# Optimization experiments

Measured on AMD Instinct MI355X. Metric: run time of the kernel, lower is better.

Reference implementation:

```python
import jax, jax.numpy as jnp
import numpy as np

DIRECTIONS = [(0, 0), (1, 0), (-1, 0), (0, 1), (0, -1)]  # (dx, dy)
BN_EPS = 1e-5


def shift2d(x, directions=DIRECTIONS):
    # x: (B, C, H, W). Split channels into G groups, roll each spatially,
    # zero out the wrapped-around border (zero_pad mode), then concat.
    C = x.shape[1]
    G = len(directions)
    base = C // G
    sizes = [base] * (G - 1) + [C - base * (G - 1)]
    starts = np.concatenate([[0], np.cumsum(sizes)])
    out = []
    for i, (dx, dy) in enumerate(directions):
        chunk = x[:, starts[i]:starts[i + 1]]
        if dx == 0 and dy == 0:
            out.append(chunk)
            continue
        y = jnp.roll(chunk, shift=(dy, dx), axis=(-2, -1))
        if dy > 0:
            y = y.at[..., :dy, :].set(0.0)
        elif dy < 0:
            y = y.at[..., dy:, :].set(0.0)
        if dx > 0:
            y = y.at[..., :, :dx].set(0.0)
        elif dx < 0:
            y = y.at[..., :, dx:].set(0.0)
        out.append(y)
    return jnp.concatenate(out, axis=1)


def setup_inputs() -> dict:
    key = jax.random.key(0)
    k1, k2, k3, k4 = jax.random.split(key, 4)
    B, Cin, Cout, H, W = 32, 256, 256, 56, 56
    x = jax.random.normal(k1, (B, Cin, H, W), dtype=jnp.float32)
    pw_w = jax.random.normal(k2, (Cout, Cin), dtype=jnp.float32) * (1.0 / np.sqrt(Cin))
    gamma = jnp.ones((Cout,), dtype=jnp.float32)
    beta = jnp.zeros((Cout,), dtype=jnp.float32)
    running_mean = jax.random.normal(k3, (Cout,), dtype=jnp.float32) * 0.1
    running_var = jax.random.uniform(k4, (Cout,), dtype=jnp.float32, minval=0.5, maxval=1.5)
    return {"x": x, "pw_w": pw_w, "gamma": gamma, "beta": beta,
            "running_mean": running_mean, "running_var": running_var}


def reference(x, pw_w, gamma, beta, running_mean, running_var):
    # Shift (parameter-free spatial mixing)
    y = shift2d(x)
    # stride=1 -> down is Identity
    # 1x1 conv (no bias): pointwise channel mixing
    y = jnp.einsum('bchw,oc->bohw', y, pw_w)
    # BatchNorm2d (inference form with running stats) + ReLU
    inv = gamma * jax.lax.rsqrt(running_var + BN_EPS)
    y = y * inv[None, :, None, None] + (beta - running_mean * inv)[None, :, None, None]
    return jax.nn.relu(y)
```

## Files before the change

kernel.cpp:

```cpp
#include <hip/hip_runtime.h>

#define H_ 56
#define W_ 56
#define HW_ 3136
#define CIN_ 256
#define COUT_ 256

typedef __attribute__((ext_vector_type(8))) short short8;
typedef __attribute__((ext_vector_type(4))) float f32x4;

__device__ unsigned short g_wbf[COUT_ * CIN_];

__device__ __forceinline__ unsigned short f2bf(float f) {
  union { float f; unsigned int i; } v; v.f = f;
  unsigned int b = v.i + (0x7fffu + ((v.i >> 16) & 1u));
  return (unsigned short)(b >> 16);
}

__global__ __launch_bounds__(256)
void prep_weights(const float* __restrict__ wgt) {
  int idx  = blockIdx.x * 256 + threadIdx.x;
  int j    = idx & 7;
  int lane = (idx >> 3) & 63;
  int b    = (idx >> 9) & 3;
  int ks   = (idx >> 11) & 7;
  int wo   = (idx >> 14) & 1;
  int bo   = idx >> 15;
  int o = bo * 128 + wo * 64 + b * 16 + (lane & 15);
  int k = ks * 32 + j * 4 + (lane >> 4);
  g_wbf[idx] = f2bf(wgt[o * CIN_ + k]);
}

__global__ __launch_bounds__(256, 4)
void shiftconv_gemm(const float* __restrict__ x,
                    const float* __restrict__ gamma,
                    const float* __restrict__ beta,
                    const float* __restrict__ rmean,
                    const float* __restrict__ rvar,
                    float* __restrict__ out)
{
  __shared__ float bnp[256];
  __shared__ float tbuf[4][32 * 33];

  const int t = threadIdx.x;
  const int orig = blockIdx.x;
  const int wgid = (orig & 7) * 392 + (orig >> 3);
  const int bo   = wgid & 1;
  const int bn   = wgid >> 1;

  const int lane = t & 63;
  const int wv   = t >> 6;
  const int wn   = wv & 1;
  const int wo   = wv >> 1;
  const int quad = lane >> 4;
  const int l15  = lane & 15;

  if (t < 128) {
    int o = bo * 128 + t;
    float inv = gamma[o] * rsqrtf(rvar[o] + 1e-5f);
    bnp[2 * t]     = inv;
    bnp[2 * t + 1] = beta[o] - rmean[o] * inv;
  }
  __syncthreads();

  const int nglob0 = bn * 64;
  const int bidx   = nglob0 / HW_;
  const int rem    = nglob0 - bidx * HW_;
  const int hw0    = rem + wn * 32 + l15;
  const int hh0    = hw0 / W_;
  const int ww0    = hw0 - hh0 * W_;
  const int hw1    = hw0 + 16;
  const int hh1    = hw1 / W_;
  const int ww1    = hw1 - hh1 * W_;

  const int qh = quad * HW_;
  const unsigned int base0 = (unsigned int)((hw0 + qh) * 4);
  const unsigned int base1 = (unsigned int)((hw1 + qh) * 4);
  const bool v0L = (ww0 >= 1),      v1L = (ww1 >= 1);
  const bool v0R = (ww0 <= W_ - 2), v1R = (ww1 <= W_ - 2);
  const bool v0U = (hh0 >= 1),      v1U = (hh1 >= 1);
  const bool v0D = (hh0 <= H_ - 2), v1D = (hh1 <= H_ - 2);
  unsigned int vo0[5], vo1[5];
  vo0[0] = base0;                                               vo1[0] = base1;
  vo0[1] = v0L ? (unsigned int)((hw0 - 1  + qh) * 4) : base0;   vo1[1] = v1L ? (unsigned int)((hw1 - 1  + qh) * 4) : base1;
  vo0[2] = v0R ? (unsigned int)((hw0 + 1  + qh) * 4) : base0;   vo1[2] = v1R ? (unsigned int)((hw1 + 1  + qh) * 4) : base1;
  vo0[3] = v0U ? (unsigned int)((hw0 - W_ + qh) * 4) : base0;   vo1[3] = v1U ? (unsigned int)((hw1 - W_ + qh) * 4) : base1;
  vo0[4] = v0D ? (unsigned int)((hw0 + W_ + qh) * 4) : base0;   vo1[4] = v1D ? (unsigned int)((hw1 + W_ + qh) * 4) : base1;
  float fm0[5], fm1[5];
  fm0[0] = 1.f;               fm1[0] = 1.f;
  fm0[1] = v0L ? 1.f : 0.f;   fm1[1] = v1L ? 1.f : 0.f;
  fm0[2] = v0R ? 1.f : 0.f;   fm1[2] = v1R ? 1.f : 0.f;
  fm0[3] = v0U ? 1.f : 0.f;   fm1[3] = v1U ? 1.f : 0.f;
  fm0[4] = v0D ? 1.f : 0.f;   fm1[4] = v1D ? 1.f : 0.f;

  const char* __restrict__ px = (const char*)(x + (size_t)bidx * CIN_ * HW_);
  const unsigned short* __restrict__ wp =
      g_wbf + (size_t)(bo * 2 + wo) * 16384 + lane * 8;

  f32x4 acc[2][4];
  #pragma unroll
  for (int a = 0; a < 2; ++a)
    #pragma unroll
    for (int b = 0; b < 4; ++b)
      acc[a][b] = (f32x4){0.f, 0.f, 0.f, 0.f};

  #pragma unroll
  for (int ks = 0; ks < 8; ++ks) {
    short8 wf[4];
    #pragma unroll
    for (int b = 0; b < 4; ++b)
      wf[b] = *(const short8*)(wp + ks * 2048 + b * 512);

    float fa0[8], fa1[8];
    #pragma unroll
    for (int j = 0; j < 8; ++j) {
      const int c0 = ks * 32 + 4 * j;
      unsigned int o0, o1; float m0, m1;
      if (c0 == 48)       { bool hi = quad >= 3;
        o0 = hi ? vo0[1] : vo0[0]; o1 = hi ? vo1[1] : vo1[0];
        m0 = hi ? fm0[1] : 1.f;    m1 = hi ? fm1[1] : 1.f; }
      else if (c0 == 100) { bool hi = quad >= 2;
        o0 = hi ? vo0[2] : vo0[1]; o1 = hi ? vo1[2] : vo1[1];
        m0 = hi ? fm0[2] : fm0[1]; m1 = hi ? fm1[2] : fm1[1]; }
      else if (c0 == 152) { bool hi = quad >= 1;
        o0 = hi ? vo0[3] : vo0[2]; o1 = hi ? vo1[3] : vo1[2];
        m0 = hi ? fm0[3] : fm0[2]; m1 = hi ? fm1[3] : fm1[2]; }
      else {
        const int r = (c0 >= 51) + (c0 >= 102) + (c0 >= 153) + (c0 >= 204);
        o0 = vo0[r]; o1 = vo1[r]; m0 = fm0[r]; m1 = fm1[r];
      }
      const unsigned int cb = (unsigned int)(c0 * HW_ * 4);
      float v0 = *(const float*)(px + (o0 + cb));
      float v1 = *(const float*)(px + (o1 + cb));
      fa0[j] = v0 * m0;
      fa1[j] = v1 * m1;
    }

    union { short8 v; unsigned int d[4]; } af0, af1;
    #pragma unroll
    for (int jj = 0; jj < 4; ++jj) {
      asm("v_cvt_pk_bf16_f32 %0, %1, %2" : "=v"(af0.d[jj]) : "v"(fa0[2*jj]), "v"(fa0[2*jj+1]));
      asm("v_cvt_pk_bf16_f32 %0, %1, %2" : "=v"(af1.d[jj]) : "v"(fa1[2*jj]), "v"(fa1[2*jj+1]));
    }

    #pragma unroll
    for (int b = 0; b < 4; ++b) {
      acc[0][b] = __builtin_amdgcn_mfma_f32_16x16x32_bf16(af0.v, wf[b], acc[0][b], 0, 0, 0);
      acc[1][b] = __builtin_amdgcn_mfma_f32_16x16x32_bf16(af1.v, wf[b], acc[1][b], 0, 0, 0);
    }
  }

  float invb[4], addb[4];
  #pragma unroll
  for (int b = 0; b < 4; ++b) {
    int ol = wo * 64 + b * 16 + l15;
    invb[b] = bnp[2 * ol];
    addb[b] = bnp[2 * ol + 1];
  }
  float* tb = &tbuf[wv][0];
  const size_t obase0 = (size_t)bidx * COUT_ * HW_;
  #pragma unroll
  for (int hb = 0; hb < 2; ++hb) {
    #pragma unroll
    for (int bb = 0; bb < 2; ++bb) {
      const int b = hb * 2 + bb;
      #pragma unroll
      for (int a = 0; a < 2; ++a)
        #pragma unroll
        for (int r = 0; r < 4; ++r) {
          float v = fmaxf(fmaf(acc[a][b][r], invb[b], addb[b]), 0.f);
          tb[(bb * 16 + l15) * 33 + (a * 16 + quad * 4 + r)] = v;
        }
    }
    asm volatile("s_waitcnt lgkmcnt(0)" ::: "memory");
    #pragma unroll
    for (int oi = 0; oi < 16; ++oi) {
      int ol  = oi * 2 + (lane >> 5);
      int nl  = lane & 31;
      float v = tb[ol * 33 + nl];
      int og  = bo * 128 + wo * 64 + hb * 32 + ol;
      int hwg = rem + wn * 32 + nl;
      out[obase0 + (size_t)og * HW_ + hwg] = v;
    }
    asm volatile("s_waitcnt lgkmcnt(0)" ::: "memory");
  }
}

extern "C" void kernel_launch(void* const* d_in, const int* in_sizes, int n_in,
                              void* d_out, int out_size, void* d_ws, size_t ws_size,
                              hipStream_t stream) {
  const float* x     = (const float*)d_in[0];
  const float* wgt   = (const float*)d_in[1];
  const float* gamma = (const float*)d_in[2];
  const float* beta  = (const float*)d_in[3];
  const float* rmean = (const float*)d_in[4];
  const float* rvar  = (const float*)d_in[5];
  float* out = (float*)d_out;

  prep_weights<<<dim3(256), dim3(256), 0, stream>>>(wgt);
  shiftconv_gemm<<<dim3(3136), dim3(256), 0, stream>>>(x, gamma, beta, rmean, rvar, out);
}
```

Measured before the change: 231.7 us.

## Stage block weight slice in LDS and double spatial tile per 512-thread block

Each block now covers 128 output channels by 128 spatial positions with 8 waves instead of 64 positions with 4 waves. The 64KB bf16 weight slice is loaded once per block into shared memory using direct global-to-LDS loads, replacing per-wave global weight reads inside the K loop. Tiles may now span batch boundaries, so each lane computes its own batch index. The epilogue transpose buffer reuses the weight LDS region. The cost is 64KB+ of LDS per block, which limits occupancy, plus an extra barrier.

```diff
diff --git a/kernel.cpp b/kernel.cpp
--- a/kernel.cpp
+++ b/kernel.cpp
@@ -17,21 +17,26 @@
   return (unsigned short)(b >> 16);
 }
 
+__device__ __forceinline__ void gload_lds16(const unsigned short* g, unsigned short* l) {
+  __builtin_amdgcn_global_load_lds(
+      (const __attribute__((address_space(1))) unsigned int*)g,
+      (__attribute__((address_space(3))) unsigned int*)l, 16, 0, 0);
+}
+
 __global__ __launch_bounds__(256)
 void prep_weights(const float* __restrict__ wgt) {
   int idx  = blockIdx.x * 256 + threadIdx.x;
   int j    = idx & 7;
   int lane = (idx >> 3) & 63;
-  int b    = (idx >> 9) & 3;
-  int ks   = (idx >> 11) & 7;
-  int wo   = (idx >> 14) & 1;
-  int bo   = idx >> 15;
-  int o = bo * 128 + wo * 64 + b * 16 + (lane & 15);
+  int obg  = (idx >> 9) & 7;
+  int ks   = (idx >> 12) & 7;
+  int bm   = idx >> 15;
+  int o = bm * 128 + obg * 16 + (lane & 15);
   int k = ks * 32 + j * 4 + (lane >> 4);
   g_wbf[idx] = f2bf(wgt[o * CIN_ + k]);
 }
 
-__global__ __launch_bounds__(256, 4)
+__global__ __launch_bounds__(512, 4)
 void shiftconv_gemm(const float* __restrict__ x,
                     const float* __restrict__ gamma,
                     const float* __restrict__ beta,
@@ -39,53 +44,55 @@
                     const float* __restrict__ rvar,
                     float* __restrict__ out)
 {
+  __shared__ unsigned short Wlds[128 * 256];
   __shared__ float bnp[256];
-  __shared__ float tbuf[4][32 * 33];
 
   const int t = threadIdx.x;
   const int orig = blockIdx.x;
-  const int wgid = (orig & 7) * 392 + (orig >> 3);
-  const int bo   = wgid & 1;
-  const int bn   = wgid >> 1;
+  const int wgid = (orig & 7) * 196 + (orig >> 3);
+  const int bm    = wgid & 1;
+  const int chunk = wgid >> 1;
 
   const int lane = t & 63;
   const int wv   = t >> 6;
-  const int wn   = wv & 1;
-  const int wo   = wv >> 1;
+  const int wo   = wv >> 2;
+  const int wn   = wv & 3;
   const int quad = lane >> 4;
   const int l15  = lane & 15;
 
   if (t < 128) {
-    int o = bo * 128 + t;
+    int o = bm * 128 + t;
     float inv = gamma[o] * rsqrtf(rvar[o] + 1e-5f);
     bnp[2 * t]     = inv;
     bnp[2 * t + 1] = beta[o] - rmean[o] * inv;
   }
-  __syncthreads();
-
-  const int nglob0 = bn * 64;
-  const int bidx   = nglob0 / HW_;
-  const int rem    = nglob0 - bidx * HW_;
-  const int hw0    = rem + wn * 32 + l15;
-  const int hh0    = hw0 / W_;
-  const int ww0    = hw0 - hh0 * W_;
-  const int hw1    = hw0 + 16;
-  const int hh1    = hw1 / W_;
-  const int ww1    = hw1 - hh1 * W_;
-
-  const int qh = quad * HW_;
-  const unsigned int base0 = (unsigned int)((hw0 + qh) * 4);
-  const unsigned int base1 = (unsigned int)((hw1 + qh) * 4);
+
+  {
+    const unsigned short* g = g_wbf + bm * 32768 + t * 8;
+    unsigned short* l = &Wlds[t * 8];
+    #pragma unroll
+    for (int p = 0; p < 8; ++p)
+      gload_lds16(g + p * 4096, l + p * 4096);
+  }
+
+  const int ng0 = chunk * 128 + wn * 32 + l15;
+  const int ng1 = ng0 + 16;
+  const int bi0 = ng0 / HW_, rn0 = ng0 - bi0 * HW_;
+  const int bi1 = ng1 / HW_, rn1 = ng1 - bi1 * HW_;
+  const int hh0 = rn0 / W_,  ww0 = rn0 - hh0 * W_;
+  const int hh1 = rn1 / W_,  ww1 = rn1 - hh1 * W_;
+  const unsigned int eb0 = (unsigned int)(bi0 * CIN_ * HW_ + rn0 + quad * HW_);
+  const unsigned int eb1 = (unsigned int)(bi1 * CIN_ * HW_ + rn1 + quad * HW_);
   const bool v0L = (ww0 >= 1),      v1L = (ww1 >= 1);
   const bool v0R = (ww0 <= W_ - 2), v1R = (ww1 <= W_ - 2);
   const bool v0U = (hh0 >= 1),      v1U = (hh1 >= 1);
   const bool v0D = (hh0 <= H_ - 2), v1D = (hh1 <= H_ - 2);
   unsigned int vo0[5], vo1[5];
-  vo0[0] = base0;                                               vo1[0] = base1;
-  vo0[1] = v0L ? (unsigned int)((hw0 - 1  + qh) * 4) : base0;   vo1[1] = v1L ? (unsigned int)((hw1 - 1  + qh) * 4) : base1;
-  vo0[2] = v0R ? (unsigned int)((hw0 + 1  + qh) * 4) : base0;   vo1[2] = v1R ? (unsigned int)((hw1 + 1  + qh) * 4) : base1;
-  vo0[3] = v0U ? (unsigned int)((hw0 - W_ + qh) * 4) : base0;   vo1[3] = v1U ? (unsigned int)((hw1 - W_ + qh) * 4) : base1;
-  vo0[4] = v0D ? (unsigned int)((hw0 + W_ + qh) * 4) : base0;   vo1[4] = v1D ? (unsigned int)((hw1 + W_ + qh) * 4) : base1;
+  vo0[0] = eb0 * 4;                             vo1[0] = eb1 * 4;
+  vo0[1] = (v0L ? eb0 - 1   : eb0) * 4;         vo1[1] = (v1L ? eb1 - 1   : eb1) * 4;
+  vo0[2] = (v0R ? eb0 + 1   : eb0) * 4;         vo1[2] = (v1R ? eb1 + 1   : eb1) * 4;
+  vo0[3] = (v0U ? eb0 - W_  : eb0) * 4;         vo1[3] = (v1U ? eb1 - W_  : eb1) * 4;
+  vo0[4] = (v0D ? eb0 + W_  : eb0) * 4;         vo1[4] = (v1D ? eb1 + W_  : eb1) * 4;
   float fm0[5], fm1[5];
   fm0[0] = 1.f;               fm1[0] = 1.f;
   fm0[1] = v0L ? 1.f : 0.f;   fm1[1] = v1L ? 1.f : 0.f;
@@ -93,25 +100,20 @@
   fm0[3] = v0U ? 1.f : 0.f;   fm1[3] = v1U ? 1.f : 0.f;
   fm0[4] = v0D ? 1.f : 0.f;   fm1[4] = v1D ? 1.f : 0.f;
 
-  const char* __restrict__ px = (const char*)(x + (size_t)bidx * CIN_ * HW_);
-  const unsigned short* __restrict__ wp =
-      g_wbf + (size_t)(bo * 2 + wo) * 16384 + lane * 8;
-
-  f32x4 acc[2][4];
-  #pragma unroll
-  for (int a = 0; a < 2; ++a)
-    #pragma unroll
-    for (int b = 0; b < 4; ++b)
-      acc[a][b] = (f32x4){0.f, 0.f, 0.f, 0.f};
+  const char* __restrict__ px = (const char*)x;
+
+  f32x4 acc[4][2];
+  #pragma unroll
+  for (int i = 0; i < 4; ++i)
+    #pragma unroll
+    for (int j = 0; j < 2; ++j)
+      acc[i][j] = (f32x4){0.f, 0.f, 0.f, 0.f};
+
+  __syncthreads();
 
   #pragma unroll
   for (int ks = 0; ks < 8; ++ks) {
-    short8 wf[4];
-    #pragma unroll
-    for (int b = 0; b < 4; ++b)
-      wf[b] = *(const short8*)(wp + ks * 2048 + b * 512);
-
-    float fa0[8], fa1[8];
+    float fv0[8], fv1[8];
     #pragma unroll
     for (int j = 0; j < 8; ++j) {
       const int c0 = ks * 32 + 4 * j;
@@ -129,27 +131,25 @@
         const int r = (c0 >= 51) + (c0 >= 102) + (c0 >= 153) + (c0 >= 204);
         o0 = vo0[r]; o1 = vo1[r]; m0 = fm0[r]; m1 = fm1[r];
       }
-      const unsigned int cb = (unsigned int)(c0 * HW_ * 4);
-      float v0 = *(const float*)(px + (o0 + cb));
-      float v1 = *(const float*)(px + (o1 + cb));
-      fa0[j] = v0 * m0;
-      fa1[j] = v1 * m1;
-    }
-
+      const unsigned int cb = (unsigned int)(c0 * HW_) * 4u;
+      fv0[j] = *(const float*)(px + (o0 + cb)) * m0;
+      fv1[j] = *(const float*)(px + (o1 + cb)) * m1;
+    }
     union { short8 v; unsigned int d[4]; } af0, af1;
     #pragma unroll
     for (int jj = 0; jj < 4; ++jj) {
-      asm("v_cvt_pk_bf16_f32 %0, %1, %2" : "=v"(af0.d[jj]) : "v"(fa0[2*jj]), "v"(fa0[2*jj+1]));
-      asm("v_cvt_pk_bf16_f32 %0, %1, %2" : "=v"(af1.d[jj]) : "v"(fa1[2*jj]), "v"(fa1[2*jj+1]));
-    }
-
-    #pragma unroll
-    for (int b = 0; b < 4; ++b) {
-      acc[0][b] = __builtin_amdgcn_mfma_f32_16x16x32_bf16(af0.v, wf[b], acc[0][b], 0, 0, 0);
-      acc[1][b] = __builtin_amdgcn_mfma_f32_16x16x32_bf16(af1.v, wf[b], acc[1][b], 0, 0, 0);
-    }
-  }
-
+      asm("v_cvt_pk_bf16_f32 %0, %1, %2" : "=v"(af0.d[jj]) : "v"(fv0[2*jj]), "v"(fv0[2*jj+1]));
+      asm("v_cvt_pk_bf16_f32 %0, %1, %2" : "=v"(af1.d[jj]) : "v"(fv1[2*jj]), "v"(fv1[2*jj+1]));
+    }
+    #pragma unroll
+    for (int ob = 0; ob < 4; ++ob) {
+      const short8 wf = *(const short8*)(&Wlds[((ks * 8 + wo * 4 + ob) * 64 + lane) * 8]);
+      acc[ob][0] = __builtin_amdgcn_mfma_f32_16x16x32_bf16(af0.v, wf, acc[ob][0], 0, 0, 0);
+      acc[ob][1] = __builtin_amdgcn_mfma_f32_16x16x32_bf16(af1.v, wf, acc[ob][1], 0, 0, 0);
+    }
+  }
+
+  __syncthreads();
   float invb[4], addb[4];
   #pragma unroll
   for (int b = 0; b < 4; ++b) {
@@ -157,8 +157,12 @@
     invb[b] = bnp[2 * ol];
     addb[b] = bnp[2 * ol + 1];
   }
-  float* tb = &tbuf[wv][0];
-  const size_t obase0 = (size_t)bidx * COUT_ * HW_;
+  float* tb = (float*)&Wlds[0] + wv * 1056;
+  const int nl  = lane & 31;
+  const int ngs = chunk * 128 + wn * 32 + nl;
+  const int bis = ngs / HW_;
+  const int hws = ngs - bis * HW_;
+  const size_t sb = (size_t)bis * COUT_ * HW_ + hws;
   #pragma unroll
   for (int hb = 0; hb < 2; ++hb) {
     #pragma unroll
@@ -168,7 +172,7 @@
       for (int a = 0; a < 2; ++a)
         #pragma unroll
         for (int r = 0; r < 4; ++r) {
-          float v = fmaxf(fmaf(acc[a][b][r], invb[b], addb[b]), 0.f);
+          float v = fmaxf(fmaf(acc[b][a][r], invb[b], addb[b]), 0.f);
           tb[(bb * 16 + l15) * 33 + (a * 16 + quad * 4 + r)] = v;
         }
     }
@@ -176,11 +180,9 @@
     #pragma unroll
     for (int oi = 0; oi < 16; ++oi) {
       int ol  = oi * 2 + (lane >> 5);
-      int nl  = lane & 31;
       float v = tb[ol * 33 + nl];
-      int og  = bo * 128 + wo * 64 + hb * 32 + ol;
-      int hwg = rem + wn * 32 + nl;
-      out[obase0 + (size_t)og * HW_ + hwg] = v;
+      int og  = bm * 128 + wo * 64 + hb * 32 + ol;
+      out[sb + (size_t)og * HW_] = v;
     }
     asm volatile("s_waitcnt lgkmcnt(0)" ::: "memory");
   }
@@ -198,5 +200,5 @@
   float* out = (float*)d_out;
 
   prep_weights<<<dim3(256), dim3(256), 0, stream>>>(wgt);
-  shiftconv_gemm<<<dim3(3136), dim3(256), 0, stream>>>(x, gamma, beta, rmean, rvar, out);
-}
+  shiftconv_gemm<<<dim3(1568), dim3(512), 0, stream>>>(x, gamma, beta, rmean, rvar, out);
+}
```

Result: faster. 210.7 us (-9.1%).
